# Performance work log

Measured on AMD Instinct MI355X. Metric: run time of the kernel, lower is better.

## Reference

```python
import jax, jax.numpy as jnp
import numpy as np

NUM = 5          # spline intervals
KS = 3           # spline order k
GRID_LO, GRID_HI = -1.0, 1.0
KH = KW = 3      # kernel size
STRIDE = 1
PAD = 1
DIL = 1


def make_grid():
    # extended uniform grid: num+2k+1 points from lo-k*h to hi+k*h (h=(hi-lo)/num)
    h = (GRID_HI - GRID_LO) / NUM
    return GRID_LO + jnp.arange(-KS, NUM + KS + 1, dtype=jnp.float32) * h  # (12,)


def b_spline_basis(x, grid, k):
    # x: (..., ), grid: (G,) shared across features (all rows of pykan grid identical)
    # returns (..., G-1-k) Cox-de Boor bases of order k
    x = x[..., None]
    B = ((x >= grid[:-1]) & (x < grid[1:])).astype(x.dtype)
    for p in range(1, k + 1):
        left = (x - grid[:-(p + 1)]) / (grid[p:-1] - grid[:-(p + 1)]) * B[..., :-1]
        right = (grid[p + 1:] - x) / (grid[p + 1:] - grid[1:-p]) * B[..., 1:]
        B = left + right
    return B


def extract_patches(x):
    # torch.nn.Unfold ordering: (B, C, kh*kw, OH, OW), kernel positions row-major
    x = jnp.pad(x, ((0, 0), (0, 0), (PAD, PAD), (PAD, PAD)))
    B, C, H, W = x.shape
    OH = (H - DIL * (KH - 1) - 1) // STRIDE + 1
    OW = (W - DIL * (KW - 1) - 1) // STRIDE + 1
    pats = []
    for i in range(KH):
        for j in range(KW):
            pats.append(x[:, :, i * DIL:i * DIL + STRIDE * (OH - 1) + 1:STRIDE,
                          j * DIL:j * DIL + STRIDE * (OW - 1) + 1:STRIDE])
    return jnp.stack(pats, axis=2)  # (B, C, K, OH, OW)


def setup_inputs() -> dict:
    key = jax.random.key(0)
    k1, k2, k3, k4, k5 = jax.random.split(key, 5)
    B, C, O, H, W = 8, 32, 64, 32, 32
    K, M = KH * KW, NUM + KS
    x = jax.random.normal(k1, (B, C, H, W), dtype=jnp.float32)
    coef = jax.random.normal(k2, (O, C, K, M), dtype=jnp.float32) * 0.1
    scale_base = jax.random.normal(k3, (O, C, K), dtype=jnp.float32) / np.sqrt(K)
    scale_sp = jnp.ones((O, C, K), dtype=jnp.float32)
    bias = jnp.zeros((O,), dtype=jnp.float32)
    return {"x": x, "coef": coef, "scale_base": scale_base,
            "scale_sp": scale_sp, "bias": bias}


def reference(x, coef, scale_base, scale_sp, bias):
    grid = make_grid()
    p = extract_patches(x)                              # (B, C, K, OH, OW)
    B, C, K, OH, OW = p.shape
    t = p.transpose(0, 1, 3, 4, 2).reshape(B, C, OH * OW, K)  # (B, C, L, K)
    Bsp = b_spline_basis(t, grid, KS)                   # (B, C, L, K, M)
    silu = t * jax.nn.sigmoid(t)
    W_sp = scale_sp[..., None] * coef                   # (O, C, K, M)
    out = (jnp.einsum('bclk,ock->bol', silu, scale_base)
           + jnp.einsum('bclkm,ockm->bol', Bsp, W_sp))
    out = out + bias[None, :, None]
    return out.reshape(B, -1, OH, OW)
```

## Files before the change

### kernel.cpp

```cpp
#include <hip/hip_runtime.h>


typedef __attribute__((ext_vector_type(8))) short v8s;
typedef __attribute__((ext_vector_type(4))) float v4f;
typedef unsigned short ushort_t;

#define G_ELEMS   (8u * 34u * 34u * 288u)
#define WB_ELEMS  (64u * 2592u)
#define N_FEAT    (8 * 34 * 34 * 32)
#define N_TOTAL   (N_FEAT + 64 * 2592)

__device__ __forceinline__ unsigned short f2bf(float v) {
  union { float f; unsigned int u; } w; w.f = v;
  unsigned int r = w.u + 0x7FFFu + ((w.u >> 16) & 1u);
  return (unsigned short)(r >> 16);
}

__global__ __launch_bounds__(256) void kan_feat(const float* __restrict__ x,
                                                const float* __restrict__ coef,
                                                const float* __restrict__ sb,
                                                const float* __restrict__ ssp,
                                                ushort_t* __restrict__ g,
                                                ushort_t* __restrict__ Wb) {
  int tid = blockIdx.x * 256 + threadIdx.x;
  if (tid < N_FEAT) {
    int c = tid & 31;
    int cell = tid >> 5;
    int w = cell % 34;
    int hb = cell / 34;
    int h = hb % 34;
    int b = hb / 34;

    bool inb = (h >= 1) && (h <= 32) && (w >= 1) && (w <= 32);
    float t = 0.0f;
    if (inb) t = x[((b * 32 + c) * 32 + (h - 1)) * 32 + (w - 1)];

    unsigned short f0 = f2bf(t / (1.0f + __expf(-t)));
    float u  = (t + 2.2f) * 2.5f;
    float fi = floorf(u);
    int   i  = (int)fi;
    float s  = u - fi;
    float s2 = s * s, s3 = s2 * s;
    float om = 1.0f - s;
    float w0 = om * om * om * (1.0f / 6.0f);
    float w1 = (4.0f - 6.0f * s2 + 3.0f * s3) * (1.0f / 6.0f);
    float w2 = (1.0f + 3.0f * s + 3.0f * s2 - 3.0f * s3) * (1.0f / 6.0f);
    float w3 = s3 * (1.0f / 6.0f);

    ushort_t* dst = g + (size_t)cell * 288 + c;
    dst[0] = f0;
#pragma unroll
    for (int jj = 0; jj < 8; ++jj) {
      int d = jj - i + 3;
      float bv = (d == 0) ? w0 : (d == 1) ? w1 : (d == 2) ? w2 : (d == 3) ? w3 : 0.0f;
      dst[(jj + 1) * 32] = f2bf(bv);
    }
    return;
  }
  int i2 = tid - N_FEAT;
  if (i2 >= (int)WB_ELEMS) return;
  int o = i2 / 2592;
  int r = i2 - o * 2592;
  int pos = r / 288;
  int rj = r - pos * 288;
  int j = rj >> 5;
  int c = rj & 31;
  int sidx = (o * 32 + c) * 9 + pos;
  float val = (j == 0) ? sb[sidx] : ssp[sidx] * coef[sidx * 8 + (j - 1)];
  Wb[i2] = f2bf(val);
}

__global__ __launch_bounds__(256) void kan_conv(const ushort_t* __restrict__ g,
                                                const ushort_t* __restrict__ Wb,
                                                const float* __restrict__ bias,
                                                float* __restrict__ out) {
  const int lane = threadIdx.x & 63;
  const int wave = threadIdx.x >> 6;
  const int row  = lane & 15;
  const int quad = lane >> 4;
  const int mrow = blockIdx.x;
  const int b  = mrow >> 5;
  const int oh = mrow & 31;
  const int ow_base = (wave & 1) * 16;
  const int nbase   = (wave >> 1) * 32;

  const ushort_t* gb  = g + ((size_t)((b * 34 + oh) * 34 + ow_base + row)) * 288 + quad * 8;
  const ushort_t* wb0 = Wb + (size_t)(nbase + row) * 2592 + quad * 8;
  const ushort_t* wb1 = wb0 + 16 * 2592;

  v4f acc0 = {0.f, 0.f, 0.f, 0.f};
  v4f acc1 = acc0;

#pragma unroll
  for (int di = 0; di < 3; ++di) {
#pragma unroll
    for (int dj = 0; dj < 3; ++dj) {
      const ushort_t* ap  = gb + (di * 34 + dj) * 288;
      const ushort_t* bp0 = wb0 + (di * 3 + dj) * 288;
      const ushort_t* bp1 = wb1 + (di * 3 + dj) * 288;
#pragma unroll
      for (int kk = 0; kk < 9; ++kk) {
        v8s a  = *(const v8s*)(ap  + kk * 32);
        v8s b0 = *(const v8s*)(bp0 + kk * 32);
        v8s b1 = *(const v8s*)(bp1 + kk * 32);
        acc0 = __builtin_amdgcn_mfma_f32_16x16x32_bf16(a, b0, acc0, 0, 0, 0);
        acc1 = __builtin_amdgcn_mfma_f32_16x16x32_bf16(a, b1, acc1, 0, 0, 0);
      }
    }
  }

  const int o0 = nbase + row;
  const float bv0 = bias[o0];
  const float bv1 = bias[o0 + 16];
  float* p0 = out + ((size_t)(b * 64 + o0)) * 1024 + oh * 32 + ow_base + quad * 4;
  float* p1 = p0 + 16 * 1024;
  *(float4*)p0 = make_float4(acc0[0] + bv0, acc0[1] + bv0, acc0[2] + bv0, acc0[3] + bv0);
  *(float4*)p1 = make_float4(acc1[0] + bv1, acc1[1] + bv1, acc1[2] + bv1, acc1[3] + bv1);
}

extern "C" void kernel_launch(void* const* d_in, const int* in_sizes, int n_in,
                              void* d_out, int out_size, void* d_ws, size_t ws_size,
                              hipStream_t stream) {
  const float* x    = (const float*)d_in[0];
  const float* coef = (const float*)d_in[1];
  const float* sb   = (const float*)d_in[2];
  const float* ssp  = (const float*)d_in[3];
  const float* bias = (const float*)d_in[4];
  float* out = (float*)d_out;

  ushort_t* g  = (ushort_t*)d_ws;
  ushort_t* Wb = g + G_ELEMS;

  hipLaunchKernelGGL(kan_feat, dim3((N_TOTAL + 255) / 256), dim3(256), 0, stream,
                     x, coef, sb, ssp, g, Wb);
  hipLaunchKernelGGL(kan_conv, dim3(256), dim3(256), 0, stream, g, Wb, bias, out);
}
```

Measured before the change: 85.39 us.

## Split conv reduction across kernel positions with partial sums and a reduce kernel

The conv kernel now parallelizes over the 9 kernel positions (split-K), launching 128x9 blocks that each compute a 64-pixel by 64-output tile for a single position and write fp32 partials to workspace. A new reduce kernel sums the 9 partials, adds the bias and writes the output. This raises the block count from 256 to 1152 to fill more compute units and shortens each block's serial MFMA chain. In exchange it adds roughly 18 MB of partial-sum traffic and a third kernel launch.

```diff
diff --git a/kernel.cpp b/kernel.cpp
--- a/kernel.cpp
+++ b/kernel.cpp
@@ -9,6 +9,7 @@
 #define WB_ELEMS  (64u * 2592u)
 #define N_FEAT    (8 * 34 * 34 * 32)
 #define N_TOTAL   (N_FEAT + 64 * 2592)
+#define PART_STRIDE 524288u
 
 __device__ __forceinline__ unsigned short f2bf(float v) {
   union { float f; unsigned int u; } w; w.f = v;
@@ -72,50 +73,76 @@
 
 __global__ __launch_bounds__(256) void kan_conv(const ushort_t* __restrict__ g,
                                                 const ushort_t* __restrict__ Wb,
-                                                const float* __restrict__ bias,
-                                                float* __restrict__ out) {
+                                                float* __restrict__ part) {
   const int lane = threadIdx.x & 63;
   const int wave = threadIdx.x >> 6;
   const int row  = lane & 15;
   const int quad = lane >> 4;
-  const int mrow = blockIdx.x;
-  const int b  = mrow >> 5;
-  const int oh = mrow & 31;
-  const int ow_base = (wave & 1) * 16;
-  const int nbase   = (wave >> 1) * 32;
+  const int mbase = blockIdx.x * 64;
+  const int pos   = blockIdx.y;
+  const int di = pos / 3, dj = pos - di * 3;
 
-  const ushort_t* gb  = g + ((size_t)((b * 34 + oh) * 34 + ow_base + row)) * 288 + quad * 8;
-  const ushort_t* wb0 = Wb + (size_t)(nbase + row) * 2592 + quad * 8;
-  const ushort_t* wb1 = wb0 + 16 * 2592;
+  const int b   = mbase >> 10;
+  const int oh0 = (mbase & 1023) >> 5;
+  const int obase = wave * 16;
+
+  const ushort_t* wp = Wb + (size_t)(obase + row) * 2592 + pos * 288 + quad * 8;
+
+  const ushort_t* gp[4];
+#pragma unroll
+  for (int mseg = 0; mseg < 4; ++mseg) {
+    int ohs = oh0 + (mseg >> 1) + di;
+    int ows = (mseg & 1) * 16 + row + dj;
+    gp[mseg] = g + (size_t)((b * 34 + ohs) * 34 + ows) * 288 + quad * 8;
+  }
 
   v4f acc0 = {0.f, 0.f, 0.f, 0.f};
-  v4f acc1 = acc0;
+  v4f acc1 = acc0, acc2 = acc0, acc3 = acc0;
 
 #pragma unroll
-  for (int di = 0; di < 3; ++di) {
-#pragma unroll
-    for (int dj = 0; dj < 3; ++dj) {
-      const ushort_t* ap  = gb + (di * 34 + dj) * 288;
-      const ushort_t* bp0 = wb0 + (di * 3 + dj) * 288;
-      const ushort_t* bp1 = wb1 + (di * 3 + dj) * 288;
-#pragma unroll
-      for (int kk = 0; kk < 9; ++kk) {
-        v8s a  = *(const v8s*)(ap  + kk * 32);
-        v8s b0 = *(const v8s*)(bp0 + kk * 32);
-        v8s b1 = *(const v8s*)(bp1 + kk * 32);
-        acc0 = __builtin_amdgcn_mfma_f32_16x16x32_bf16(a, b0, acc0, 0, 0, 0);
-        acc1 = __builtin_amdgcn_mfma_f32_16x16x32_bf16(a, b1, acc1, 0, 0, 0);
-      }
-    }
+  for (int kk = 0; kk < 9; ++kk) {
+    v8s wf = *(const v8s*)(wp + kk * 32);
+    v8s g0 = *(const v8s*)(gp[0] + kk * 32);
+    v8s g1 = *(const v8s*)(gp[1] + kk * 32);
+    v8s g2 = *(const v8s*)(gp[2] + kk * 32);
+    v8s g3 = *(const v8s*)(gp[3] + kk * 32);
+    acc0 = __builtin_amdgcn_mfma_f32_16x16x32_bf16(wf, g0, acc0, 0, 0, 0);
+    acc1 = __builtin_amdgcn_mfma_f32_16x16x32_bf16(wf, g1, acc1, 0, 0, 0);
+    acc2 = __builtin_amdgcn_mfma_f32_16x16x32_bf16(wf, g2, acc2, 0, 0, 0);
+    acc3 = __builtin_amdgcn_mfma_f32_16x16x32_bf16(wf, g3, acc3, 0, 0, 0);
   }
 
-  const int o0 = nbase + row;
-  const float bv0 = bias[o0];
-  const float bv1 = bias[o0 + 16];
-  float* p0 = out + ((size_t)(b * 64 + o0)) * 1024 + oh * 32 + ow_base + quad * 4;
-  float* p1 = p0 + 16 * 1024;
-  *(float4*)p0 = make_float4(acc0[0] + bv0, acc0[1] + bv0, acc0[2] + bv0, acc0[3] + bv0);
-  *(float4*)p1 = make_float4(acc1[0] + bv1, acc1[1] + bv1, acc1[2] + bv1, acc1[3] + bv1);
+  float* pb = part + (size_t)pos * PART_STRIDE
+            + (size_t)(obase + quad * 4) * 8192 + mbase + row;
+#pragma unroll
+  for (int r = 0; r < 4; ++r) {
+    float* pr = pb + (size_t)r * 8192;
+    pr[0]  = acc0[r];
+    pr[16] = acc1[r];
+    pr[32] = acc2[r];
+    pr[48] = acc3[r];
+  }
+}
+
+__global__ __launch_bounds__(256) void kan_reduce(const float* __restrict__ part,
+                                                  const float* __restrict__ bias,
+                                                  float* __restrict__ out) {
+  int tid = blockIdx.x * 256 + threadIdx.x;
+  int flat = tid * 4;
+  int o = flat >> 13;
+  int l = flat & 8191;
+  int b = l >> 10;
+  int pix = l & 1023;
+
+  float4 s = *(const float4*)(part + flat);
+#pragma unroll
+  for (int ks = 1; ks < 9; ++ks) {
+    float4 p = *(const float4*)(part + (size_t)ks * PART_STRIDE + flat);
+    s.x += p.x; s.y += p.y; s.z += p.z; s.w += p.w;
+  }
+  float bv = bias[o];
+  s.x += bv; s.y += bv; s.z += bv; s.w += bv;
+  *(float4*)(out + (size_t)(b * 64 + o) * 1024 + pix) = s;
 }
 
 extern "C" void kernel_launch(void* const* d_in, const int* in_sizes, int n_in,
@@ -128,10 +155,12 @@
   const float* bias = (const float*)d_in[4];
   float* out = (float*)d_out;
 
-  ushort_t* g  = (ushort_t*)d_ws;
-  ushort_t* Wb = g + G_ELEMS;
+  ushort_t* g    = (ushort_t*)d_ws;
+  ushort_t* Wb   = g + G_ELEMS;
+  float*    part = (float*)(Wb + WB_ELEMS);
 
   hipLaunchKernelGGL(kan_feat, dim3((N_TOTAL + 255) / 256), dim3(256), 0, stream,
                      x, coef, sb, ssp, g, Wb);
-  hipLaunchKernelGGL(kan_conv, dim3(256), dim3(256), 0, stream, g, Wb, bias, out);
+  hipLaunchKernelGGL(kan_conv, dim3(128, 9), dim3(256), 0, stream, g, Wb, part);
+  hipLaunchKernelGGL(kan_reduce, dim3(512), dim3(256), 0, stream, part, bias, out);
 }
```

Measured after the change: 96.92 us. 13.5% more time.

## Fuse spline feature computation into conv kernel via LDS with split-K reduction

Applied to the files above, without the earlier changes.

Feature expansion (SiLU and cubic B-spline weights) now runs inside the conv kernel. Each block builds the three padded input rows in LDS, so the large bf16 feature tensor is no longer written to and re-read from global memory. The conv splits the 81-step K loop across four wave groups and sums their partial results in LDS. It also doubles the grid and swaps MFMA operand roles so each wave covers 32 output columns for 16 channels. In exchange, every block recomputes features that neighbouring rows share (about 3x redundant work) and adds extra barriers for the LDS reduction.

```diff
diff --git a/kernel.cpp b/kernel.cpp
--- a/kernel.cpp
+++ b/kernel.cpp
@@ -5,10 +5,9 @@
 typedef __attribute__((ext_vector_type(4))) float v4f;
 typedef unsigned short ushort_t;
 
-#define G_ELEMS   (8u * 34u * 34u * 288u)
-#define WB_ELEMS  (64u * 2592u)
-#define N_FEAT    (8 * 34 * 34 * 32)
-#define N_TOTAL   (N_FEAT + 64 * 2592)
+#define WB_ELEMS    (64u * 2592u)
+#define CELL_STRIDE 296
+#define ROW_STRIDE  (34 * CELL_STRIDE)
 
 __device__ __forceinline__ unsigned short f2bf(float v) {
   union { float f; unsigned int u; } w; w.f = v;
@@ -16,106 +15,141 @@
   return (unsigned short)(r >> 16);
 }
 
-__global__ __launch_bounds__(256) void kan_feat(const float* __restrict__ x,
-                                                const float* __restrict__ coef,
+__global__ __launch_bounds__(256) void kan_prep(const float* __restrict__ coef,
                                                 const float* __restrict__ sb,
                                                 const float* __restrict__ ssp,
-                                                ushort_t* __restrict__ g,
                                                 ushort_t* __restrict__ Wb) {
-  int tid = blockIdx.x * 256 + threadIdx.x;
-  if (tid < N_FEAT) {
-    int c = tid & 31;
-    int cell = tid >> 5;
-    int w = cell % 34;
-    int hb = cell / 34;
-    int h = hb % 34;
-    int b = hb / 34;
-
-    bool inb = (h >= 1) && (h <= 32) && (w >= 1) && (w <= 32);
-    float t = 0.0f;
-    if (inb) t = x[((b * 32 + c) * 32 + (h - 1)) * 32 + (w - 1)];
-
-    unsigned short f0 = f2bf(t / (1.0f + __expf(-t)));
-    float u  = (t + 2.2f) * 2.5f;
-    float fi = floorf(u);
-    int   i  = (int)fi;
-    float s  = u - fi;
-    float s2 = s * s, s3 = s2 * s;
-    float om = 1.0f - s;
-    float w0 = om * om * om * (1.0f / 6.0f);
-    float w1 = (4.0f - 6.0f * s2 + 3.0f * s3) * (1.0f / 6.0f);
-    float w2 = (1.0f + 3.0f * s + 3.0f * s2 - 3.0f * s3) * (1.0f / 6.0f);
-    float w3 = s3 * (1.0f / 6.0f);
-
-    ushort_t* dst = g + (size_t)cell * 288 + c;
-    dst[0] = f0;
-#pragma unroll
-    for (int jj = 0; jj < 8; ++jj) {
-      int d = jj - i + 3;
-      float bv = (d == 0) ? w0 : (d == 1) ? w1 : (d == 2) ? w2 : (d == 3) ? w3 : 0.0f;
-      dst[(jj + 1) * 32] = f2bf(bv);
-    }
-    return;
-  }
-  int i2 = tid - N_FEAT;
-  if (i2 >= (int)WB_ELEMS) return;
-  int o = i2 / 2592;
-  int r = i2 - o * 2592;
+  int i = blockIdx.x * 256 + threadIdx.x;
+  if (i >= (int)WB_ELEMS) return;
+  int o = i / 2592;
+  int r = i - o * 2592;
   int pos = r / 288;
   int rj = r - pos * 288;
   int j = rj >> 5;
   int c = rj & 31;
   int sidx = (o * 32 + c) * 9 + pos;
   float val = (j == 0) ? sb[sidx] : ssp[sidx] * coef[sidx * 8 + (j - 1)];
-  Wb[i2] = f2bf(val);
+  Wb[i] = f2bf(val);
 }
 
-__global__ __launch_bounds__(256) void kan_conv(const ushort_t* __restrict__ g,
-                                                const ushort_t* __restrict__ Wb,
-                                                const float* __restrict__ bias,
-                                                float* __restrict__ out) {
-  const int lane = threadIdx.x & 63;
-  const int wave = threadIdx.x >> 6;
+template <int LO, int HI>
+__device__ __forceinline__ void kloop(const ushort_t* __restrict__ fb,
+                                      const ushort_t* __restrict__ wp,
+                                      v4f& acc0, v4f& acc1) {
+#pragma unroll
+  for (int s = LO; s < HI; ++s) {
+    const int di = s / 27;
+    const int dj = (s / 9) % 3;
+    const int kk = s % 9;
+    const int fo = di * ROW_STRIDE + dj * CELL_STRIDE + kk * 32;
+    v8s wf = *(const v8s*)(wp + s * 32);
+    v8s a0 = *(const v8s*)(fb + fo);
+    v8s a1 = *(const v8s*)(fb + fo + 16 * CELL_STRIDE);
+    acc0 = __builtin_amdgcn_mfma_f32_16x16x32_bf16(wf, a0, acc0, 0, 0, 0);
+    acc1 = __builtin_amdgcn_mfma_f32_16x16x32_bf16(wf, a1, acc1, 0, 0, 0);
+  }
+}
+
+__global__ __launch_bounds__(512, 4) void kan_fused(const float* __restrict__ x,
+                                                    const ushort_t* __restrict__ Wb,
+                                                    const float* __restrict__ bias,
+                                                    float* __restrict__ out) {
+  __shared__ ushort_t feat[3 * ROW_STRIDE];
+  __shared__ float xs[32 * 33];
+
+  const int tid = threadIdx.x;
+  const int bx = blockIdx.x;
+  const int ohalf = bx & 1;
+  const int oh = (bx >> 1) & 31;
+  const int b = bx >> 6;
+
+  for (int r = 0; r < 3; ++r) {
+    const int h = oh + r - 1;
+    const bool hval = (h >= 0) && (h < 32);
+    if (hval) {
+      int idx = tid * 2;
+      int c = idx >> 5, w = idx & 31;
+      float2 v = *(const float2*)(x + (((b * 32 + c) * 32 + h) * 32 + w));
+      xs[c * 33 + w] = v.x;
+      xs[c * 33 + w + 1] = v.y;
+    }
+    __syncthreads();
+    for (int idx = tid; idx < 1088; idx += 512) {
+      int c = idx & 31, cell = idx >> 5;
+      int wi = cell - 1;
+      float t = 0.0f;
+      if (hval && wi >= 0 && wi < 32) t = xs[c * 33 + wi];
+
+      unsigned short f0 = f2bf(t / (1.0f + __expf(-t)));
+      float u  = (t + 2.2f) * 2.5f;
+      float fi = floorf(u);
+      int   i  = (int)fi;
+      float s  = u - fi;
+      float s2 = s * s, s3 = s2 * s;
+      float om = 1.0f - s;
+      float w0 = om * om * om * (1.0f / 6.0f);
+      float w1 = (4.0f - 6.0f * s2 + 3.0f * s3) * (1.0f / 6.0f);
+      float w2 = (1.0f + 3.0f * s + 3.0f * s2 - 3.0f * s3) * (1.0f / 6.0f);
+      float w3 = s3 * (1.0f / 6.0f);
+
+      ushort_t* dst = feat + r * ROW_STRIDE + cell * CELL_STRIDE + c;
+      dst[0] = f0;
+#pragma unroll
+      for (int jj = 0; jj < 8; ++jj) {
+        int d = jj - i + 3;
+        float bv = (d == 0) ? w0 : (d == 1) ? w1 : (d == 2) ? w2 : (d == 3) ? w3 : 0.0f;
+        dst[(jj + 1) * 32] = f2bf(bv);
+      }
+    }
+    __syncthreads();
+  }
+
+  const int wv   = tid >> 6;
+  const int lane = tid & 63;
   const int row  = lane & 15;
   const int quad = lane >> 4;
-  const int mrow = blockIdx.x;
-  const int b  = mrow >> 5;
-  const int oh = mrow & 31;
-  const int ow_base = (wave & 1) * 16;
-  const int nbase   = (wave >> 1) * 32;
+  const int og   = wv & 1;
+  const int kq   = wv >> 1;
+  const int obase = ohalf * 32 + og * 16;
 
-  const ushort_t* gb  = g + ((size_t)((b * 34 + oh) * 34 + ow_base + row)) * 288 + quad * 8;
-  const ushort_t* wb0 = Wb + (size_t)(nbase + row) * 2592 + quad * 8;
-  const ushort_t* wb1 = wb0 + 16 * 2592;
+  const ushort_t* fb = feat + row * CELL_STRIDE + quad * 8;
+  const ushort_t* wp = Wb + (size_t)(obase + row) * 2592 + quad * 8;
 
   v4f acc0 = {0.f, 0.f, 0.f, 0.f};
   v4f acc1 = acc0;
 
+  if (kq == 0)      kloop<0, 20>(fb, wp, acc0, acc1);
+  else if (kq == 1) kloop<20, 40>(fb, wp, acc0, acc1);
+  else if (kq == 2) kloop<40, 60>(fb, wp, acc0, acc1);
+  else              kloop<60, 81>(fb, wp, acc0, acc1);
+
+  __syncthreads();
+  float* red = (float*)feat;
+  if (kq != 0) {
+    float* rp = red + ((kq - 1) * 2 + og) * 512 + quad * 4 * 32 + row;
 #pragma unroll
-  for (int di = 0; di < 3; ++di) {
-#pragma unroll
-    for (int dj = 0; dj < 3; ++dj) {
-      const ushort_t* ap  = gb + (di * 34 + dj) * 288;
-      const ushort_t* bp0 = wb0 + (di * 3 + dj) * 288;
-      const ushort_t* bp1 = wb1 + (di * 3 + dj) * 288;
-#pragma unroll
-      for (int kk = 0; kk < 9; ++kk) {
-        v8s a  = *(const v8s*)(ap  + kk * 32);
-        v8s b0 = *(const v8s*)(bp0 + kk * 32);
-        v8s b1 = *(const v8s*)(bp1 + kk * 32);
-        acc0 = __builtin_amdgcn_mfma_f32_16x16x32_bf16(a, b0, acc0, 0, 0, 0);
-        acc1 = __builtin_amdgcn_mfma_f32_16x16x32_bf16(a, b1, acc1, 0, 0, 0);
-      }
+    for (int r = 0; r < 4; ++r) {
+      rp[r * 32]      = acc0[r];
+      rp[r * 32 + 16] = acc1[r];
     }
   }
-
-  const int o0 = nbase + row;
-  const float bv0 = bias[o0];
-  const float bv1 = bias[o0 + 16];
-  float* p0 = out + ((size_t)(b * 64 + o0)) * 1024 + oh * 32 + ow_base + quad * 4;
-  float* p1 = p0 + 16 * 1024;
-  *(float4*)p0 = make_float4(acc0[0] + bv0, acc0[1] + bv0, acc0[2] + bv0, acc0[3] + bv0);
-  *(float4*)p1 = make_float4(acc1[0] + bv1, acc1[1] + bv1, acc1[2] + bv1, acc1[3] + bv1);
+  __syncthreads();
+  if (kq == 0) {
+    float* o0 = out + ((size_t)(b * 64 + obase + quad * 4)) * 1024 + oh * 32 + row;
+#pragma unroll
+    for (int r = 0; r < 4; ++r) {
+      float bv = bias[obase + quad * 4 + r];
+      float s0 = acc0[r], s1 = acc1[r];
+#pragma unroll
+      for (int gs = 0; gs < 3; ++gs) {
+        const float* rp = red + (gs * 2 + og) * 512 + (quad * 4 + r) * 32 + row;
+        s0 += rp[0];
+        s1 += rp[16];
+      }
+      o0[(size_t)r * 1024]      = s0 + bv;
+      o0[(size_t)r * 1024 + 16] = s1 + bv;
+    }
+  }
 }
 
 extern "C" void kernel_launch(void* const* d_in, const int* in_sizes, int n_in,
@@ -128,10 +162,8 @@
   const float* bias = (const float*)d_in[4];
   float* out = (float*)d_out;
 
-  ushort_t* g  = (ushort_t*)d_ws;
-  ushort_t* Wb = g + G_ELEMS;
+  ushort_t* Wb = (ushort_t*)d_ws;
 
-  hipLaunchKernelGGL(kan_feat, dim3((N_TOTAL + 255) / 256), dim3(256), 0, stream,
-                     x, coef, sb, ssp, g, Wb);
-  hipLaunchKernelGGL(kan_conv, dim3(256), dim3(256), 0, stream, g, Wb, bias, out);
+  hipLaunchKernelGGL(kan_prep, dim3(648), dim3(256), 0, stream, coef, sb, ssp, Wb);
+  hipLaunchKernelGGL(kan_fused, dim3(512), dim3(512), 0, stream, x, Wb, bias, out);
 }
```

Result: faster. 83.67 us (-2.0%).
